# Kernel tuning notes

Measured on AMD Instinct MI355X. Metric: run time of the kernel, lower is better.

The kernel has to match this reference:

```python
import jax, jax.numpy as jnp
import numpy as np

DIM = 1024
HEADS = 16
DIM_HEAD = 64
INNER = HEADS * DIM_HEAD  # 1024


def setup_inputs() -> dict:
    key = jax.random.key(0)
    kx, kqkv, kwo, kbo = jax.random.split(key, 4)
    x = jax.random.normal(kx, (4, 2048, DIM), dtype=jnp.float32)
    # nn.Linear weights stored as [out, in]; we keep [in, out] for x @ W
    w_qkv = jax.random.normal(kqkv, (DIM, 3 * INNER), dtype=jnp.float32) * (1.0 / np.sqrt(DIM))
    w_out = jax.random.normal(kwo, (INNER, DIM), dtype=jnp.float32) * (1.0 / np.sqrt(INNER))
    b_out = jax.random.normal(kbo, (DIM,), dtype=jnp.float32) * 0.01
    return {"x": x, "w_qkv": w_qkv, "w_out": w_out, "b_out": b_out}


def reference(x, w_qkv, w_out, b_out):
    b, n, _ = x.shape
    scale = 1.0 / np.sqrt(DIM_HEAD)
    qkv = x @ w_qkv  # [b, n, 3*inner]
    q, k, v = jnp.split(qkv, 3, axis=-1)
    # [b, n, inner] -> [b, h, n, d]
    reshape = lambda z: z.reshape(b, n, HEADS, DIM_HEAD).transpose(0, 2, 1, 3)
    q, k, v = reshape(q), reshape(k), reshape(v)
    sim = jnp.einsum('bhid,bhjd->bhij', q, k) * scale
    attn = jax.nn.softmax(sim, axis=-1)  # dropout p=0.0 -> identity
    out = jnp.einsum('bhij,bhjd->bhid', attn, v)
    out = out.transpose(0, 2, 1, 3).reshape(b, n, INNER)
    return out @ w_out + b_out
```

## Files before the change

### kernel.cpp

```cpp
#include <hip/hip_runtime.h>
#include <hip/hip_fp16.h>

typedef __attribute__((ext_vector_type(4))) float f32x4;
typedef __attribute__((ext_vector_type(8))) _Float16 h8;
typedef __attribute__((ext_vector_type(4))) _Float16 h4;
typedef __attribute__((ext_vector_type(2))) _Float16 h2;
typedef __attribute__((ext_vector_type(2))) __fp16 fp16x2;

__device__ __forceinline__ void gld16(const _Float16* g, _Float16* l) {
  __builtin_amdgcn_global_load_lds(
      (const __attribute__((address_space(1))) void*)g,
      (__attribute__((address_space(3))) void*)l, 16, 0, 0);
}

__device__ __forceinline__ h4 pack4(float p0, float p1, float p2, float p3) {
  fp16x2 lo = __builtin_amdgcn_cvt_pkrtz(p0, p1);
  fp16x2 hi = __builtin_amdgcn_cvt_pkrtz(p2, p3);
  h2 lo2 = __builtin_bit_cast(h2, lo);
  h2 hi2 = __builtin_bit_cast(h2, hi);
  return __builtin_shufflevector(lo2, hi2, 0, 1, 2, 3);
}

__global__ void cvt_f32_h(const float* __restrict__ in, _Float16* __restrict__ out, int n8) {
  for (int i = blockIdx.x * blockDim.x + threadIdx.x; i < n8; i += gridDim.x * blockDim.x) {
    const f32x4* p = (const f32x4*)(in + (size_t)i * 8);
    f32x4 a = p[0], b = p[1];
    h8 o;
    o[0] = (_Float16)a[0]; o[1] = (_Float16)a[1]; o[2] = (_Float16)a[2]; o[3] = (_Float16)a[3];
    o[4] = (_Float16)b[0]; o[5] = (_Float16)b[1]; o[6] = (_Float16)b[2]; o[7] = (_Float16)b[3];
    *(h8*)(out + (size_t)i * 8) = o;
  }
}

__global__ void transpose_cvt(const float* __restrict__ in, _Float16* __restrict__ out, int R, int C) {
  __shared__ float tile[32][33];
  const int tx = threadIdx.x & 31, ty = threadIdx.x >> 5;
  const int c = blockIdx.x * 32 + tx;
#pragma unroll
  for (int j = 0; j < 32; j += 8) {
    int r = blockIdx.y * 32 + ty + j;
    tile[ty + j][tx] = in[(size_t)r * C + c];
  }
  __syncthreads();
#pragma unroll
  for (int j = 0; j < 32; j += 8) {
    out[(size_t)(blockIdx.x * 32 + ty + j) * R + blockIdx.y * 32 + tx] = (_Float16)tile[tx][ty + j];
  }
}

template <int EPI>
__global__ __launch_bounds__(256, 2)
void gemm_kernel(const _Float16* __restrict__ A, const _Float16* __restrict__ Bt,
                 float* __restrict__ outF, const float* __restrict__ bias,
                 _Float16* __restrict__ q_h, _Float16* __restrict__ k_h,
                 _Float16* __restrict__ v_t, const int Nn, const int K) {
  __shared__ _Float16 As[128 * 64];
  __shared__ _Float16 Bs[128 * 64];
  const int tid = threadIdx.x;
  const int wid = tid >> 6, lane = tid & 63;
  const int g = lane >> 4, r16 = lane & 15;
  const int wr = wid >> 1, wc = wid & 1;
  const int row0 = blockIdx.x * 128;
  const int col0 = blockIdx.y * 128;
  f32x4 acc[4][4] = {};
  const int sr = tid >> 3, sc = tid & 7;
  const _Float16* ag = A + (size_t)(row0 + sr) * K + sc * 8;
  const _Float16* bg = Bt + (size_t)(col0 + sr) * K + sc * 8;

  for (int kt = 0; kt < K; kt += 64) {
    __syncthreads();
#pragma unroll
    for (int i = 0; i < 4; ++i)
      gld16(ag + (size_t)i * 32 * K + kt, As + i * 2048 + wid * 512);
#pragma unroll
    for (int i = 0; i < 4; ++i)
      gld16(bg + (size_t)i * 32 * K + kt, Bs + i * 2048 + wid * 512);
    __syncthreads();

#pragma unroll
    for (int kk = 0; kk < 2; ++kk) {
      h8 af[4], bf[4];
#pragma unroll
      for (int mt = 0; mt < 4; ++mt)
        af[mt] = *(const h8*)(As + (wr * 64 + mt * 16 + r16) * 64 + kk * 32 + g * 8);
#pragma unroll
      for (int nt = 0; nt < 4; ++nt)
        bf[nt] = *(const h8*)(Bs + (wc * 64 + nt * 16 + r16) * 64 + kk * 32 + g * 8);
#pragma unroll
      for (int mt = 0; mt < 4; ++mt)
#pragma unroll
        for (int nt = 0; nt < 4; ++nt)
          acc[mt][nt] = __builtin_amdgcn_mfma_f32_16x16x32_f16(af[mt], bf[nt], acc[mt][nt], 0, 0, 0);
    }
  }

  if (EPI == 0) {
    const float qscale = 0.125f * 1.44269504088896340736f;
#pragma unroll
    for (int mt = 0; mt < 4; ++mt) {
#pragma unroll
      for (int nt = 0; nt < 4; ++nt) {
        const int j = col0 + wc * 64 + nt * 16 + r16;
        const int which = j >> 10;
        const int hd = j & 1023;
        const int hh = hd >> 6, dd = hd & 63;
#pragma unroll
        for (int rg = 0; rg < 4; ++rg) {
          const int mm = row0 + wr * 64 + mt * 16 + g * 4 + rg;
          const int b = mm >> 11, n = mm & 2047;
          const size_t bh = (size_t)(b * 16 + hh);
          const float v = acc[mt][nt][rg];
          if (which == 0)      q_h[(bh * 2048 + n) * 64 + dd] = (_Float16)(v * qscale);
          else if (which == 1) k_h[(bh * 2048 + n) * 64 + dd] = (_Float16)v;
          else                 v_t[(bh * 64 + dd) * 2048 + n] = (_Float16)v;
        }
      }
    }
  } else {
#pragma unroll
    for (int mt = 0; mt < 4; ++mt) {
#pragma unroll
      for (int nt = 0; nt < 4; ++nt) {
        const int j = col0 + wc * 64 + nt * 16 + r16;
        const float bv = bias[j];
#pragma unroll
        for (int rg = 0; rg < 4; ++rg) {
          const int mm = row0 + wr * 64 + mt * 16 + g * 4 + rg;
          outF[(size_t)mm * Nn + j] = acc[mt][nt][rg] + bv;
        }
      }
    }
  }
}

__device__ __forceinline__ void stage_kv(const _Float16* Kg, const _Float16* Vg,
                                         _Float16* KsB, _Float16* VsB,
                                         int kv0, int sr, int sc8, int wid) {
#pragma unroll
  for (int i = 0; i < 2; ++i) {
    int r = i * 32 + sr;
    gld16(Kg + (size_t)(kv0 + r) * 64 + (sc8 ^ ((r & 7) * 8)), KsB + i * 2048 + wid * 512);
    gld16(Vg + (size_t)r * 2048 + kv0 + (sc8 ^ ((r & 7) * 8)), VsB + i * 2048 + wid * 512);
  }
}

__global__ __launch_bounds__(256, 2)
void attn_kernel(const _Float16* __restrict__ Qall, const _Float16* __restrict__ Kall,
                 const _Float16* __restrict__ Vtall, _Float16* __restrict__ Oall) {
  __shared__ _Float16 smem[2][2][64 * 64];
  const int tid = threadIdx.x;
  const int wid = tid >> 6, lane = tid & 63;
  const int g = lane >> 4, r16 = lane & 15;
  const int blk = (blockIdx.x & 7) * 64 + (blockIdx.x >> 3);
  const int qt = blk & 7;
  const int bh = blk >> 3;
  const _Float16* Qg = Qall + (size_t)bh * (2048 * 64);
  const _Float16* Kg = Kall + (size_t)bh * (2048 * 64);
  const _Float16* Vg = Vtall + (size_t)bh * (2048 * 64);
  const int q0 = qt * 256;
  const int sr = tid >> 3, sc8 = (tid & 7) * 8;

  h8 qf[4][2];
#pragma unroll
  for (int qb = 0; qb < 4; ++qb) {
    const int qrow = q0 + wid * 64 + qb * 16 + r16;
#pragma unroll
    for (int kd = 0; kd < 2; ++kd)
      qf[qb][kd] = *(const h8*)(Qg + (size_t)qrow * 64 + kd * 32 + g * 8);
  }
  stage_kv(Kg, Vg, smem[0][0], smem[0][1], 0, sr, sc8, wid);
  __syncthreads();

  f32x4 ot[4][4] = {};
  float m[4], l[4];
#pragma unroll
  for (int qb = 0; qb < 4; ++qb) { m[qb] = -3.0e38f; l[qb] = 0.f; }

  auto compute = [&](const _Float16* KsB, const _Float16* VsB) {
    h8 kf[4][2];
#pragma unroll
    for (int kb = 0; kb < 4; ++kb) {
      const int krow = kb * 16 + r16;
#pragma unroll
      for (int kd = 0; kd < 2; ++kd)
        kf[kb][kd] = *(const h8*)(KsB + krow * 64 + ((kd * 32 + g * 8) ^ ((krow & 7) * 8)));
    }
    h4 vf[4][4];
#pragma unroll
    for (int db = 0; db < 4; ++db) {
      const int vrow = db * 16 + r16;
#pragma unroll
      for (int kg = 0; kg < 4; ++kg)
        vf[db][kg] = *(const h4*)(VsB + vrow * 64 + ((kg * 16 + g * 4) ^ ((vrow & 7) * 8)));
    }
#pragma unroll
    for (int qb = 0; qb < 4; ++qb) {
      f32x4 st[4];
      __builtin_amdgcn_s_setprio(1);
#pragma unroll
      for (int kb = 0; kb < 4; ++kb) {
        f32x4 z = {};
        st[kb] = __builtin_amdgcn_mfma_f32_16x16x32_f16(kf[kb][0], qf[qb][0], z, 0, 0, 0);
      }
#pragma unroll
      for (int kb = 0; kb < 4; ++kb)
        st[kb] = __builtin_amdgcn_mfma_f32_16x16x32_f16(kf[kb][1], qf[qb][1], st[kb], 0, 0, 0);
      __builtin_amdgcn_s_setprio(0);

      float a0 = fmaxf(fmaxf(st[0][0], st[0][1]), fmaxf(st[0][2], st[0][3]));
      float a1 = fmaxf(fmaxf(st[1][0], st[1][1]), fmaxf(st[1][2], st[1][3]));
      float a2 = fmaxf(fmaxf(st[2][0], st[2][1]), fmaxf(st[2][2], st[2][3]));
      float a3 = fmaxf(fmaxf(st[3][0], st[3][1]), fmaxf(st[3][2], st[3][3]));
      float pmax = fmaxf(fmaxf(a0, a1), fmaxf(a2, a3));
      pmax = fmaxf(pmax, __shfl_xor(pmax, 16));
      pmax = fmaxf(pmax, __shfl_xor(pmax, 32));
      if (__any(pmax > m[qb] + 8.f)) {
        const float mn = fmaxf(m[qb], pmax);
        const float corr = __builtin_amdgcn_exp2f(m[qb] - mn);
        l[qb] *= corr;
#pragma unroll
        for (int db = 0; db < 4; ++db) ot[qb][db] *= corr;
        m[qb] = mn;
      }
      float rs = 0.f;
      h4 pb[4];
#pragma unroll
      for (int kb = 0; kb < 4; ++kb) {
        float p0 = __builtin_amdgcn_exp2f(st[kb][0] - m[qb]);
        float p1 = __builtin_amdgcn_exp2f(st[kb][1] - m[qb]);
        float p2 = __builtin_amdgcn_exp2f(st[kb][2] - m[qb]);
        float p3 = __builtin_amdgcn_exp2f(st[kb][3] - m[qb]);
        rs += (p0 + p1) + (p2 + p3);
        pb[kb] = pack4(p0, p1, p2, p3);
      }
      rs += __shfl_xor(rs, 16);
      rs += __shfl_xor(rs, 32);
      l[qb] += rs;
      __builtin_amdgcn_s_setprio(1);
#pragma unroll
      for (int kg = 0; kg < 4; ++kg)
#pragma unroll
        for (int db = 0; db < 4; ++db)
          ot[qb][db] = __builtin_amdgcn_mfma_f32_16x16x16f16(vf[db][kg], pb[kg], ot[qb][db], 0, 0, 0);
      __builtin_amdgcn_s_setprio(0);
    }
  };

#pragma unroll 1
  for (int tt = 0; tt < 16; ++tt) {
    stage_kv(Kg, Vg, smem[1][0], smem[1][1], (tt * 2 + 1) * 64, sr, sc8, wid);
    compute(smem[0][0], smem[0][1]);
    __syncthreads();
    if (tt < 15) stage_kv(Kg, Vg, smem[0][0], smem[0][1], (tt * 2 + 2) * 64, sr, sc8, wid);
    compute(smem[1][0], smem[1][1]);
    __syncthreads();
  }

  _Float16* olds = &smem[0][0][0];
#pragma unroll
  for (int qb = 0; qb < 4; ++qb) {
    const float inv = 1.f / l[qb];
    const int qrow = wid * 64 + qb * 16 + r16;
    const int x = (qrow & 7) * 8;
#pragma unroll
    for (int db = 0; db < 4; ++db) {
      h4 o;
#pragma unroll
      for (int rg = 0; rg < 4; ++rg) o[rg] = (_Float16)(ot[qb][db][rg] * inv);
      *(h4*)(olds + qrow * 64 + ((db * 16 + g * 4) ^ x)) = o;
    }
  }
  __syncthreads();
  const int bb = bh >> 4, hh = bh & 15;
#pragma unroll
  for (int i = 0; i < 8; ++i) {
    const int idx = tid + i * 256;
    const int q = idx >> 3, c = idx & 7;
    h8 vv = *(const h8*)(olds + q * 64 + ((c * 8) ^ ((q & 7) * 8)));
    *(h8*)(Oall + ((size_t)(bb * 2048 + q0 + q) * 1024 + hh * 64 + c * 8)) = vv;
  }
}

extern "C" void kernel_launch(void* const* d_in, const int* in_sizes, int n_in,
                              void* d_out, int out_size, void* d_ws, size_t ws_size,
                              hipStream_t stream) {
  const float* x     = (const float*)d_in[0];
  const float* w_qkv = (const float*)d_in[1];
  const float* w_out = (const float*)d_in[2];
  const float* b_out = (const float*)d_in[3];
  float* out = (float*)d_out;

  char* ws = (char*)d_ws;
  _Float16* x_h    = (_Float16*)(ws);
  _Float16* wqkv_t = (_Float16*)(ws + 16777216);
  _Float16* wout_t = (_Float16*)(ws + 23068672);
  _Float16* q_h    = (_Float16*)(ws + 25165824);
  _Float16* k_h    = (_Float16*)(ws + 41943040);
  _Float16* v_t    = (_Float16*)(ws + 58720256);
  _Float16* o_h    = (_Float16*)(ws + 75497472);

  hipLaunchKernelGGL(cvt_f32_h, dim3(2048), dim3(256), 0, stream, x, x_h, (8192 * 1024) / 8);
  hipLaunchKernelGGL(transpose_cvt, dim3(96, 32), dim3(256), 0, stream, w_qkv, wqkv_t, 1024, 3072);
  hipLaunchKernelGGL(transpose_cvt, dim3(32, 32), dim3(256), 0, stream, w_out, wout_t, 1024, 1024);

  hipLaunchKernelGGL((gemm_kernel<0>), dim3(64, 24), dim3(256), 0, stream,
                     x_h, wqkv_t, nullptr, nullptr, q_h, k_h, v_t, 3072, 1024);

  hipLaunchKernelGGL(attn_kernel, dim3(512), dim3(256), 0, stream, q_h, k_h, v_t, o_h);

  hipLaunchKernelGGL((gemm_kernel<1>), dim3(64, 8), dim3(256), 0, stream,
                     o_h, wout_t, out, b_out, nullptr, nullptr, nullptr, 1024, 1024);
}
```

Measured before the change: 230.2 us.

## Split attention KV range across two blocks and merge partial outputs

Each (batch, head, query-tile) now runs in two blocks, and each block handles half of the key/value sequence. Each block writes an unnormalized-then-normalized partial output plus its row max and sum. A new combine kernel rescales the two partials with log-sum-exp weights and writes the final head-interleaved output. The aim is more parallelism in the attention stage, paid for by an extra launch, extra global traffic for the partials, and workspace buffers reused from earlier stages.

New measurement: 239.2 us. 3.9% more time.

```diff
diff --git a/kernel.cpp b/kernel.cpp
--- a/kernel.cpp
+++ b/kernel.cpp
@@ -146,18 +146,22 @@
 
 __global__ __launch_bounds__(256, 2)
 void attn_kernel(const _Float16* __restrict__ Qall, const _Float16* __restrict__ Kall,
-                 const _Float16* __restrict__ Vtall, _Float16* __restrict__ Oall) {
+                 const _Float16* __restrict__ Vtall,
+                 _Float16* __restrict__ opart0, _Float16* __restrict__ opart1,
+                 float2* __restrict__ lm0, float2* __restrict__ lm1) {
   __shared__ _Float16 smem[2][2][64 * 64];
   const int tid = threadIdx.x;
   const int wid = tid >> 6, lane = tid & 63;
   const int g = lane >> 4, r16 = lane & 15;
-  const int blk = (blockIdx.x & 7) * 64 + (blockIdx.x >> 3);
+  const int blk = (blockIdx.x & 7) * 128 + (blockIdx.x >> 3);
   const int qt = blk & 7;
-  const int bh = blk >> 3;
+  const int p  = (blk >> 3) & 1;
+  const int bh = blk >> 4;
   const _Float16* Qg = Qall + (size_t)bh * (2048 * 64);
   const _Float16* Kg = Kall + (size_t)bh * (2048 * 64);
   const _Float16* Vg = Vtall + (size_t)bh * (2048 * 64);
   const int q0 = qt * 256;
+  const int kvb = p * 1024;
   const int sr = tid >> 3, sc8 = (tid & 7) * 8;
 
   h8 qf[4][2];
@@ -168,7 +172,7 @@
     for (int kd = 0; kd < 2; ++kd)
       qf[qb][kd] = *(const h8*)(Qg + (size_t)qrow * 64 + kd * 32 + g * 8);
   }
-  stage_kv(Kg, Vg, smem[0][0], smem[0][1], 0, sr, sc8, wid);
+  stage_kv(Kg, Vg, smem[0][0], smem[0][1], kvb, sr, sc8, wid);
   __syncthreads();
 
   f32x4 ot[4][4] = {};
@@ -247,13 +251,21 @@
   };
 
 #pragma unroll 1
-  for (int tt = 0; tt < 16; ++tt) {
-    stage_kv(Kg, Vg, smem[1][0], smem[1][1], (tt * 2 + 1) * 64, sr, sc8, wid);
+  for (int tt = 0; tt < 8; ++tt) {
+    stage_kv(Kg, Vg, smem[1][0], smem[1][1], kvb + (tt * 2 + 1) * 64, sr, sc8, wid);
     compute(smem[0][0], smem[0][1]);
     __syncthreads();
-    if (tt < 15) stage_kv(Kg, Vg, smem[0][0], smem[0][1], (tt * 2 + 2) * 64, sr, sc8, wid);
+    if (tt < 7) stage_kv(Kg, Vg, smem[0][0], smem[0][1], kvb + (tt * 2 + 2) * 64, sr, sc8, wid);
     compute(smem[1][0], smem[1][1]);
     __syncthreads();
+  }
+
+  _Float16* op  = p ? opart1 : opart0;
+  float2*   lmp = p ? lm1 : lm0;
+  if (lane < 16) {
+#pragma unroll
+    for (int qb = 0; qb < 4; ++qb)
+      lmp[bh * 2048 + q0 + wid * 64 + qb * 16 + r16] = make_float2(m[qb], l[qb]);
   }
 
   _Float16* olds = &smem[0][0][0];
@@ -271,14 +283,34 @@
     }
   }
   __syncthreads();
-  const int bb = bh >> 4, hh = bh & 15;
 #pragma unroll
   for (int i = 0; i < 8; ++i) {
     const int idx = tid + i * 256;
     const int q = idx >> 3, c = idx & 7;
     h8 vv = *(const h8*)(olds + q * 64 + ((c * 8) ^ ((q & 7) * 8)));
-    *(h8*)(Oall + ((size_t)(bb * 2048 + q0 + q) * 1024 + hh * 64 + c * 8)) = vv;
-  }
+    *(h8*)(op + ((size_t)(bh * 2048 + q0 + q) * 64 + c * 8)) = vv;
+  }
+}
+
+__global__ void combine_o(const _Float16* __restrict__ op0, const _Float16* __restrict__ op1,
+                          const float2* __restrict__ lm0, const float2* __restrict__ lm1,
+                          _Float16* __restrict__ Oall) {
+  const int idx = blockIdx.x * 256 + threadIdx.x;
+  const int row = idx >> 3, c = idx & 7;
+  const int bh = row >> 11, q = row & 2047;
+  const int b = bh >> 4, h = bh & 15;
+  const float2 a0 = lm0[row], a1 = lm1[row];
+  const float M = fmaxf(a0.x, a1.x);
+  float w0 = a0.y * __builtin_amdgcn_exp2f(a0.x - M);
+  float w1 = a1.y * __builtin_amdgcn_exp2f(a1.x - M);
+  const float inv = 1.f / (w0 + w1);
+  w0 *= inv; w1 *= inv;
+  h8 v0 = *(const h8*)(op0 + (size_t)row * 64 + c * 8);
+  h8 v1 = *(const h8*)(op1 + (size_t)row * 64 + c * 8);
+  h8 o;
+#pragma unroll
+  for (int j = 0; j < 8; ++j) o[j] = (_Float16)(w0 * (float)v0[j] + w1 * (float)v1[j]);
+  *(h8*)(Oall + ((size_t)(b * 2048 + q) * 1024 + h * 64 + c * 8)) = o;
 }
 
 extern "C" void kernel_launch(void* const* d_in, const int* in_sizes, int n_in,
@@ -298,6 +330,10 @@
   _Float16* k_h    = (_Float16*)(ws + 41943040);
   _Float16* v_t    = (_Float16*)(ws + 58720256);
   _Float16* o_h    = (_Float16*)(ws + 75497472);
+  _Float16* opart0 = x_h;
+  _Float16* opart1 = (_Float16*)(ws + 92274688);
+  float2*   lm0    = (float2*)(ws + 16777216);
+  float2*   lm1    = (float2*)(ws + 16777216 + 1048576);
 
   hipLaunchKernelGGL(cvt_f32_h, dim3(2048), dim3(256), 0, stream, x, x_h, (8192 * 1024) / 8);
   hipLaunchKernelGGL(transpose_cvt, dim3(96, 32), dim3(256), 0, stream, w_qkv, wqkv_t, 1024, 3072);
@@ -306,7 +342,10 @@
   hipLaunchKernelGGL((gemm_kernel<0>), dim3(64, 24), dim3(256), 0, stream,
                      x_h, wqkv_t, nullptr, nullptr, q_h, k_h, v_t, 3072, 1024);
 
-  hipLaunchKernelGGL(attn_kernel, dim3(512), dim3(256), 0, stream, q_h, k_h, v_t, o_h);
+  hipLaunchKernelGGL(attn_kernel, dim3(1024), dim3(256), 0, stream,
+                     q_h, k_h, v_t, opart0, opart1, lm0, lm1);
+  hipLaunchKernelGGL(combine_o, dim3(4096), dim3(256), 0, stream,
+                     opart0, opart1, lm0, lm1, o_h);
 
   hipLaunchKernelGGL((gemm_kernel<1>), dim3(64, 8), dim3(256), 0, stream,
                      o_h, wout_t, out, b_out, nullptr, nullptr, nullptr, 1024, 1024);
```
